# Performance work log

Hardware: AMD Instinct MI355X
Metric: run time of the kernel (lower is better)

Reference implementation:

```python
import jax, jax.numpy as jnp
import numpy as np

B, S, D_MODEL, N_HEADS = 2, 2048, 1024, 16
HEAD_DIM = D_MODEL // N_HEADS
BASE = 10000.0

# 3D RoPE slice sizes: n_pairs = head_dim//2 split into x,y,z
_n_pairs = HEAD_DIM // 2
_px = _n_pairs // 3
_py = _n_pairs // 3
_pz = _n_pairs - _px - _py
D_X, D_Y, D_Z = _px * 2, _py * 2, _pz * 2  # 20, 20, 24


def _rotate_half(x):
    # interleaved pairs: (x0,x1,x2,x3,...) -> (-x1,x0,-x3,x2,...)
    x1 = x[..., ::2]
    x2 = x[..., 1::2]
    return jnp.stack((-x2, x1), axis=-1).reshape(x.shape)


def _rope_apply(x, pos, dim):
    # x: [B,H,S,dim]; pos: [B,S] int coords
    if dim == 0:
        return x
    inv_freq = 1.0 / (BASE ** (jnp.arange(0, dim, 2, dtype=jnp.float32) / dim))
    t = pos.astype(jnp.float32)[..., None] * inv_freq          # [B,S,dim//2]
    cos = jnp.repeat(jnp.cos(t), 2, axis=-1)[:, None]          # [B,1,S,dim]
    sin = jnp.repeat(jnp.sin(t), 2, axis=-1)[:, None]
    return x * cos + _rotate_half(x) * sin


def _rope3d(q, k, pos_xyz):
    s1, s2, s3 = D_X, D_X + D_Y, D_X + D_Y + D_Z
    parts_q, parts_k = [], []
    for (a, b), ax in (((0, s1), 0), ((s1, s2), 1), ((s2, s3), 2)):
        d = b - a
        parts_q.append(_rope_apply(q[..., a:b], pos_xyz[..., ax], d))
        parts_k.append(_rope_apply(k[..., a:b], pos_xyz[..., ax], d))
    return jnp.concatenate(parts_q, axis=-1), jnp.concatenate(parts_k, axis=-1)


def setup_inputs() -> dict:
    key = jax.random.key(0)
    k1, k2, k3, k4 = jax.random.split(key, 4)
    hidden_states = jax.random.normal(k1, (B, S, D_MODEL), dtype=jnp.float32)
    # padding: each batch row keeps first `len` tokens
    lengths = jnp.array([S - 37, S - 130], dtype=jnp.int32)
    attention_mask = jnp.arange(S)[None, :] < lengths[:, None]          # [B,S] bool, True=keep
    causal_mask = jnp.triu(jnp.ones((S, S), dtype=bool), k=1)[None, None]  # True=masked
    pos_xyz = jax.random.randint(k2, (B, S, 3), 0, 30).astype(jnp.int32)
    w_qkv = jax.random.normal(k3, (3 * D_MODEL, D_MODEL), dtype=jnp.float32) * (D_MODEL ** -0.5)
    w_out = jax.random.normal(k4, (D_MODEL, D_MODEL), dtype=jnp.float32) * (D_MODEL ** -0.5)
    return {"hidden_states": hidden_states, "w_qkv": w_qkv, "w_out": w_out,
            "attention_mask": attention_mask, "causal_mask": causal_mask,
            "pos_xyz": pos_xyz}


def reference(hidden_states, w_qkv, w_out, attention_mask, causal_mask, pos_xyz):
    Bb, Ss, Dd = hidden_states.shape
    scale = HEAD_DIM ** -0.5
    qkv = jnp.einsum('bsd,ed->bse', hidden_states, w_qkv)               # [B,S,3D]
    qkv = qkv.reshape(Bb, Ss, 3, N_HEADS, HEAD_DIM).transpose(2, 0, 3, 1, 4)
    q, k, v = qkv[0], qkv[1], qkv[2]                                    # [B,H,S,hd]
    q, k = _rope3d(q, k, pos_xyz)
    scores = jnp.einsum('bhqd,bhkd->bhqk', q, k) * scale                # [B,H,S,S]
    scores = jnp.where(causal_mask, -jnp.inf, scores)
    scores = jnp.where(attention_mask[:, None, None, :], scores, -jnp.inf)
    weights = jax.nn.softmax(scores, axis=-1)                           # dropout p=0 (eval)
    out = jnp.einsum('bhqk,bhkd->bhqd', weights, v)
    out = out.transpose(0, 2, 1, 3).reshape(Bb, Ss, Dd)
    return jnp.einsum('bsd,ed->bse', out, w_out)
```

## Files before the change

### kernel.cpp

```cpp
#include <hip/hip_runtime.h>
#include <math.h>

extern "C" __device__ float __ocml_native_exp2_f32(float);

namespace {

typedef __attribute__((ext_vector_type(8))) short short8;
typedef __attribute__((ext_vector_type(4))) short short4b;
typedef __attribute__((ext_vector_type(4))) float floatx4;

constexpr int B_ = 2;
constexpr int S_ = 2048;
constexpr int DM_ = 1024;
constexpr int NH_ = 16;
constexpr int HD_ = 64;

__device__ inline unsigned short f2bf(float f) {
  unsigned u = __builtin_bit_cast(unsigned, f);
  u += 0x7fffu + ((u >> 16) & 1u);
  return (unsigned short)(u >> 16);
}

template <int CTRL>
__device__ inline float dpp_ror(float x) {
  const int r = __builtin_amdgcn_update_dpp(
      0, __builtin_bit_cast(int, x), CTRL, 0xF, 0xF, false);
  return __builtin_bit_cast(float, r);
}

__device__ inline void gl2lds16(const unsigned short* g, unsigned short* l) {
  __builtin_amdgcn_global_load_lds(
      (const __attribute__((address_space(1))) unsigned int*)g,
      (__attribute__((address_space(3))) unsigned int*)l, 16, 0, 0);
}

__global__ __launch_bounds__(256) void prep(
    const float* __restrict__ hidden, const float* __restrict__ wqkv,
    const float* __restrict__ wout, const unsigned char* __restrict__ mask,
    unsigned short* __restrict__ hb, int* __restrict__ lengths) {
  const int bid = blockIdx.x;
  if (bid < 4096) {
    const int i = bid * 256 + threadIdx.x;
    const float* src;
    int off;
    if (i < 524288)              { src = hidden; off = 0; }
    else if (i < 524288 + 393216){ src = wqkv;   off = 524288; }
    else                         { src = wout;   off = 524288 + 393216; }
    const size_t j = (size_t)(i - off);
    const float4 a = ((const float4*)src)[j * 2];
    const float4 b = ((const float4*)src)[j * 2 + 1];
    short8 v;
    v[0] = (short)f2bf(a.x); v[1] = (short)f2bf(a.y);
    v[2] = (short)f2bf(a.z); v[3] = (short)f2bf(a.w);
    v[4] = (short)f2bf(b.x); v[5] = (short)f2bf(b.y);
    v[6] = (short)f2bf(b.z); v[7] = (short)f2bf(b.w);
    ((short8*)hb)[i] = v;
  } else {
    const int b = bid - 4096;
    const int es1 = (mask[1] != 0);
    __shared__ int cnt;
    if (threadIdx.x == 0) cnt = 0;
    __syncthreads();
    int local = 0;
    for (int s = threadIdx.x; s < S_; s += blockDim.x) {
      bool nz;
      if (es1) nz = mask[b * S_ + s] != 0;
      else     nz = ((const unsigned int*)mask)[b * S_ + s] != 0;
      local += nz ? 1 : 0;
    }
    atomicAdd(&cnt, local);
    __syncthreads();
    if (threadIdx.x == 0) lengths[b] = cnt;
  }
}

__global__ __launch_bounds__(256) void qkv_gemm(
    const unsigned short* __restrict__ A, const unsigned short* __restrict__ W,
    const int* __restrict__ pos_xyz,
    unsigned short* __restrict__ Qb, unsigned short* __restrict__ Kb,
    unsigned short* __restrict__ Vtb) {
  __shared__ __align__(16) unsigned short As[128 * 32];
  __shared__ __align__(16) unsigned short Bs[128 * 32];
  const int m0 = blockIdx.y * 128, n0 = blockIdx.x * 128;
  const int w = threadIdx.x >> 6, lane = threadIdx.x & 63;
  const int lm = lane & 15, q4 = lane >> 4;
  const int srow = w * 32;
  const int r_in = lane >> 2, c_in = (lane & 3) * 8;
  const int wr = (w >> 1) * 64, wc = (w & 1) * 64;
  const int which = n0 >> 10;
  floatx4 acc[4][4];
  const floatx4 z4 = {0.f, 0.f, 0.f, 0.f};
#pragma unroll
  for (int i = 0; i < 4; i++)
#pragma unroll
    for (int j = 0; j < 4; j++) acc[i][j] = z4;

  for (int k0 = 0; k0 < DM_; k0 += 32) {
    gl2lds16(A + (size_t)(m0 + srow + r_in) * DM_ + k0 + c_in, As + srow * 32);
    gl2lds16(A + (size_t)(m0 + srow + 16 + r_in) * DM_ + k0 + c_in,
             As + (srow + 16) * 32);
    gl2lds16(W + (size_t)(n0 + srow + r_in) * DM_ + k0 + c_in, Bs + srow * 32);
    gl2lds16(W + (size_t)(n0 + srow + 16 + r_in) * DM_ + k0 + c_in,
             Bs + (srow + 16) * 32);
    __syncthreads();
    short8 af[4], bf[4];
#pragma unroll
    for (int t = 0; t < 4; t++)
      af[t] = *(const short8*)(As + (wr + t * 16 + lm) * 32 + q4 * 8);
#pragma unroll
    for (int t = 0; t < 4; t++)
      bf[t] = *(const short8*)(Bs + (wc + t * 16 + lm) * 32 + q4 * 8);
    if (which == 2) {
#pragma unroll
      for (int i = 0; i < 4; i++)
#pragma unroll
        for (int j = 0; j < 4; j++)
          acc[i][j] = __builtin_amdgcn_mfma_f32_16x16x32_bf16(af[i], bf[j],
                                                              acc[i][j], 0, 0, 0);
    } else {
#pragma unroll
      for (int i = 0; i < 4; i++)
#pragma unroll
        for (int j = 0; j < 4; j++)
          acc[i][j] = __builtin_amdgcn_mfma_f32_16x16x32_bf16(bf[i], af[j],
                                                              acc[i][j], 0, 0, 0);
    }
    __syncthreads();
  }

  const int h = ((n0 + wc) & 1023) >> 6;
  if (which == 2) {
#pragma unroll
    for (int nt = 0; nt < 4; nt++) {
      const int d = nt * 16 + lm;
#pragma unroll
      for (int mt = 0; mt < 4; mt++) {
        const int m = m0 + wr + mt * 16 + q4 * 4;
        const int bi = m >> 11, si = m & (S_ - 1);
        short4b pk;
#pragma unroll
        for (int r = 0; r < 4; r++) pk[r] = (short)f2bf(acc[mt][nt][r]);
        *(short4b*)(Vtb + ((size_t)(bi * NH_ + h) * HD_ + d) * S_ + si) = pk;
      }
    }
  } else {
    unsigned short* Dst = (which == 0) ? Qb : Kb;
    const float osc = (which == 0) ? 0.125f * 1.44269504088896f : 1.0f;
#pragma unroll
    for (int nt = 0; nt < 4; nt++) {
      const int dbase = nt * 16 + q4 * 4;
      const int p0 = dbase >> 1;
      int axis, j0, dseg;
      if (p0 < 10)      { axis = 0; j0 = p0;      dseg = 20; }
      else if (p0 < 20) { axis = 1; j0 = p0 - 10; dseg = 20; }
      else              { axis = 2; j0 = p0 - 20; dseg = 24; }
      const float invf0 =
          __expf(-(2.0f * (float)j0 / (float)dseg) * 9.210340371976184f);
      const float invf1 =
          __expf(-(2.0f * (float)(j0 + 1) / (float)dseg) * 9.210340371976184f);
#pragma unroll
      for (int mt = 0; mt < 4; mt++) {
        const int m = m0 + wr + mt * 16 + lm;
        const int bi = m >> 11, si = m & (S_ - 1);
        const int pos = pos_xyz[((size_t)bi * S_ + si) * 3 + axis];
        short4b pk;
#pragma unroll
        for (int u = 0; u < 2; u++) {
          const float ve = acc[nt][mt][2 * u], vo = acc[nt][mt][2 * u + 1];
          float sn, cs;
          sincosf((float)pos * (u ? invf1 : invf0), &sn, &cs);
          pk[2 * u]     = (short)f2bf(fmaf(ve, cs, -vo * sn) * osc);
          pk[2 * u + 1] = (short)f2bf(fmaf(vo, cs, ve * sn) * osc);
        }
        *(short4b*)(Dst + ((size_t)(bi * NH_ + h) * S_ + si) * HD_ + dbase) = pk;
      }
    }
  }
}

__global__ __launch_bounds__(256) void flash_mfma(
    const unsigned short* __restrict__ Q, const unsigned short* __restrict__ Kg,
    const unsigned short* __restrict__ Vt, const int* __restrict__ lengths,
    unsigned short* __restrict__ Oa) {
  __shared__ __align__(16) unsigned short Ks[2 * 64 * 64];
  __shared__ __align__(16) unsigned short Vs[2 * 64 * 64];
  __shared__ __align__(16) unsigned short Ps[4][16 * 64];

  const int lin = blockIdx.y * gridDim.x + blockIdx.x;
  const int xcd = lin & 7, k = lin >> 3;
  const int s = k >> 5, c = k & 31;
  const int pc = (c & 1) ? 31 - (c >> 1) : (c >> 1);
  const int qt = (s & 1) ? 31 - pc : pc;
  const int bh = xcd * 4 + s;
  const int b = bh >> 4, h = bh & 15;
  const int q0 = qt * 64;

  const int w = threadIdx.x >> 6, lane = threadIdx.x & 63;
  const int lm = lane & 15, q4 = lane >> 4;
  const int len = lengths[b];
  const unsigned short* Qp = Q + (size_t)bh * S_ * HD_;
  const unsigned short* Kp = Kg + (size_t)bh * S_ * HD_;
  const unsigned short* Vp = Vt + (size_t)bh * HD_ * S_;

  const int r8 = lane >> 3, c8 = lane & 7;
  const int rs0 = w * 16 + r8, rs1 = rs0 + 8;
  const int cs = (c8 ^ (rs0 & 7)) << 3;
  const unsigned short* gK0 = Kp + (size_t)rs0 * HD_ + cs;
  const unsigned short* gK1 = Kp + (size_t)rs1 * HD_ + cs;
  const unsigned short* gV0 = Vp + (size_t)rs0 * S_ + cs;
  const unsigned short* gV1 = Vp + (size_t)rs1 * S_ + cs;
  unsigned short* dK0 = Ks + w * 16 * 64;
  unsigned short* dK1 = Ks + (w * 16 + 8) * 64;
  unsigned short* dV0 = Vs + w * 16 * 64;
  unsigned short* dV1 = Vs + (w * 16 + 8) * 64;

  const int qrow = q0 + w * 16 + lm;
  short8 qf[2];
  qf[0] = *(const short8*)(Qp + (size_t)qrow * HD_ + q4 * 8);
  qf[1] = *(const short8*)(Qp + (size_t)qrow * HD_ + 32 + q4 * 8);

  const floatx4 z4 = {0.f, 0.f, 0.f, 0.f};
  floatx4 o[4];
#pragma unroll
  for (int dt = 0; dt < 4; dt++) o[dt] = z4;
  float m_i[4], l_i[4];
#pragma unroll
  for (int r = 0; r < 4; r++) { m_i[r] = -1e30f; l_i[r] = 0.0f; }

  unsigned short* ps = Ps[w];
  const int ktiles = min(qt + 1, (len + 63) >> 6);

  gl2lds16(gK0, dK0);
  gl2lds16(gK1, dK1);
  gl2lds16(gV0, dV0);
  gl2lds16(gV1, dV1);
  __syncthreads();

  int cur = 0;
  for (int kt = 0; kt < ktiles; kt++) {
    const int k0 = kt * 64;
    if (kt + 1 < ktiles) {
      const size_t koff = (size_t)(k0 + 64) * HD_;
      const int nb = (cur ^ 1) * 4096;
      gl2lds16(gK0 + koff, dK0 + nb);
      gl2lds16(gK1 + koff, dK1 + nb);
      gl2lds16(gV0 + (k0 + 64), dV0 + nb);
      gl2lds16(gV1 + (k0 + 64), dV1 + nb);
    }
    const unsigned short* kc = Ks + cur * 4096;
    const unsigned short* vc = Vs + cur * 4096;

    floatx4 sc[4];
    __builtin_amdgcn_s_setprio(1);
#pragma unroll
    for (int nt = 0; nt < 4; nt++) {
      const int row = nt * 16 + lm, sw = row & 7;
      const unsigned short* kb = kc + row * 64;
      const short8 b0 = *(const short8*)(kb + ((q4 ^ sw) << 3));
      const short8 b1 = *(const short8*)(kb + (((q4 + 4) ^ sw) << 3));
      sc[nt] = __builtin_amdgcn_mfma_f32_16x16x32_bf16(qf[0], b0, z4, 0, 0, 0);
      sc[nt] = __builtin_amdgcn_mfma_f32_16x16x32_bf16(qf[1], b1, sc[nt], 0, 0, 0);
    }
    __builtin_amdgcn_s_setprio(0);
    if (kt == qt || k0 + 64 > len) {
#pragma unroll
      for (int nt = 0; nt < 4; nt++) {
        const int col = k0 + nt * 16 + lm;
#pragma unroll
        for (int r = 0; r < 4; r++) {
          const int row = q0 + w * 16 + q4 * 4 + r;
          if (col > row || col >= len) sc[nt][r] = -1e30f;
        }
      }
    }
    float mx[4];
#pragma unroll
    for (int r = 0; r < 4; r++) {
      float m0 = fmaxf(fmaxf(sc[0][r], sc[1][r]), fmaxf(sc[2][r], sc[3][r]));
      m0 = fmaxf(m0, dpp_ror<0x121>(m0));
      m0 = fmaxf(m0, dpp_ror<0x122>(m0));
      m0 = fmaxf(m0, dpp_ror<0x124>(m0));
      m0 = fmaxf(m0, dpp_ror<0x128>(m0));
      mx[r] = m0;
    }
    const bool ok = (mx[0] <= m_i[0] + 8.f) && (mx[1] <= m_i[1] + 8.f) &&
                    (mx[2] <= m_i[2] + 8.f) && (mx[3] <= m_i[3] + 8.f);
    if (!__all(ok)) {
#pragma unroll
      for (int r = 0; r < 4; r++) {
        const float mt = fmaxf(m_i[r], mx[r]);
        const float al = __ocml_native_exp2_f32(m_i[r] - mt);
        l_i[r] *= al;
        m_i[r] = mt;
#pragma unroll
        for (int dt = 0; dt < 4; dt++) o[dt][r] *= al;
      }
    }
#pragma unroll
    for (int r = 0; r < 4; r++) {
      float rs = 0.0f;
#pragma unroll
      for (int nt = 0; nt < 4; nt++) {
        const float pp = __ocml_native_exp2_f32(sc[nt][r] - m_i[r]);
        sc[nt][r] = pp;
        rs += pp;
      }
      rs += dpp_ror<0x121>(rs);
      rs += dpp_ror<0x122>(rs);
      rs += dpp_ror<0x124>(rs);
      rs += dpp_ror<0x128>(rs);
      l_i[r] += rs;
    }
#pragma unroll
    for (int nt = 0; nt < 4; nt++)
#pragma unroll
      for (int r = 0; r < 4; r++) {
        const int row = q4 * 4 + r;
        const int cc = (((nt * 2 + (lm >> 3)) ^ (row & 7)) << 3) | (lm & 7);
        ps[row * 64 + cc] = f2bf(sc[nt][r]);
      }
    __builtin_amdgcn_s_setprio(1);
#pragma unroll
    for (int ks = 0; ks < 2; ks++) {
      const short8 pf = *(const short8*)(
          ps + lm * 64 + ((((ks << 2) + q4) ^ (lm & 7)) << 3));
#pragma unroll
      for (int dt = 0; dt < 4; dt++) {
        const int row = dt * 16 + lm, sw = row & 7;
        const short8 vf = *(const short8*)(
            vc + row * 64 + ((((ks << 2) + q4) ^ sw) << 3));
        o[dt] = __builtin_amdgcn_mfma_f32_16x16x32_bf16(pf, vf, o[dt], 0, 0, 0);
      }
    }
    __builtin_amdgcn_s_setprio(0);
    __syncthreads();
    cur ^= 1;
  }
  float invl[4];
#pragma unroll
  for (int r = 0; r < 4; r++) invl[r] = 1.0f / l_i[r];
#pragma unroll
  for (int dt = 0; dt < 4; dt++)
#pragma unroll
    for (int r = 0; r < 4; r++) {
      const int row = q0 + w * 16 + q4 * 4 + r;
      const int col = h * HD_ + dt * 16 + lm;
      Oa[((size_t)b * S_ + row) * DM_ + col] = f2bf(o[dt][r] * invl[r]);
    }
}

__global__ __launch_bounds__(256) void out_gemm(
    const unsigned short* __restrict__ A, const unsigned short* __restrict__ W,
    float* __restrict__ C) {
  __shared__ __align__(16) unsigned short As[128 * 32];
  __shared__ __align__(16) unsigned short Bs[128 * 32];
  const int m0 = blockIdx.y * 128, n0 = blockIdx.x * 128;
  const int w = threadIdx.x >> 6, lane = threadIdx.x & 63;
  const int lm = lane & 15, q4 = lane >> 4;
  const int srow = w * 32;
  const int r_in = lane >> 2, c_in = (lane & 3) * 8;
  const int wr = (w >> 1) * 64, wc = (w & 1) * 64;
  floatx4 acc[4][4];
  const floatx4 z4 = {0.f, 0.f, 0.f, 0.f};
#pragma unroll
  for (int i = 0; i < 4; i++)
#pragma unroll
    for (int j = 0; j < 4; j++) acc[i][j] = z4;

  for (int k0 = 0; k0 < DM_; k0 += 32) {
    gl2lds16(A + (size_t)(m0 + srow + r_in) * DM_ + k0 + c_in, As + srow * 32);
    gl2lds16(A + (size_t)(m0 + srow + 16 + r_in) * DM_ + k0 + c_in,
             As + (srow + 16) * 32);
    gl2lds16(W + (size_t)(n0 + srow + r_in) * DM_ + k0 + c_in, Bs + srow * 32);
    gl2lds16(W + (size_t)(n0 + srow + 16 + r_in) * DM_ + k0 + c_in,
             Bs + (srow + 16) * 32);
    __syncthreads();
    short8 af[4], bf[4];
#pragma unroll
    for (int t = 0; t < 4; t++)
      af[t] = *(const short8*)(As + (wr + t * 16 + lm) * 32 + q4 * 8);
#pragma unroll
    for (int t = 0; t < 4; t++)
      bf[t] = *(const short8*)(Bs + (wc + t * 16 + lm) * 32 + q4 * 8);
#pragma unroll
    for (int i = 0; i < 4; i++)
#pragma unroll
      for (int j = 0; j < 4; j++)
        acc[i][j] =
            __builtin_amdgcn_mfma_f32_16x16x32_bf16(bf[i], af[j], acc[i][j],
                                                    0, 0, 0);
    __syncthreads();
  }
#pragma unroll
  for (int nt = 0; nt < 4; nt++) {
    const int nbase = n0 + wc + nt * 16 + q4 * 4;
#pragma unroll
    for (int mt = 0; mt < 4; mt++) {
      const int m = m0 + wr + mt * 16 + lm;
      *(floatx4*)(C + (size_t)m * DM_ + nbase) = acc[nt][mt];
    }
  }
}

}

extern "C" void kernel_launch(void* const* d_in, const int* in_sizes, int n_in,
                              void* d_out, int out_size, void* d_ws, size_t ws_size,
                              hipStream_t stream) {
  const float* hidden = (const float*)d_in[0];
  const float* w_qkv = (const float*)d_in[1];
  const float* w_out = (const float*)d_in[2];
  const unsigned char* amask = (const unsigned char*)d_in[3];
  const int* pos_xyz = (const int*)d_in[5];
  float* out = (float*)d_out;

  constexpr size_t NHID = (size_t)B_ * S_ * DM_;
  constexpr size_t NWQ = (size_t)3 * DM_ * DM_;
  constexpr size_t NWO = (size_t)DM_ * DM_;
  constexpr size_t NQKV = (size_t)B_ * NH_ * S_ * HD_;

  unsigned short* hb = (unsigned short*)d_ws;
  unsigned short* wqb = hb + NHID;
  unsigned short* wob = wqb + NWQ;
  unsigned short* Qb = wob + NWO;
  unsigned short* Kb = Qb + NQKV;
  unsigned short* Vtb = Kb + NQKV;
  unsigned short* attn = Vtb + NQKV;
  int* lens = (int*)(attn + NQKV);

  prep<<<dim3(4096 + B_), dim3(256), 0, stream>>>(hidden, w_qkv, w_out, amask,
                                                  hb, lens);
  qkv_gemm<<<dim3(3 * DM_ / 128, B_ * S_ / 128), dim3(256), 0, stream>>>(
      hb, wqb, pos_xyz, Qb, Kb, Vtb);
  flash_mfma<<<dim3(S_ / 64, B_ * NH_), dim3(256), 0, stream>>>(
      Qb, Kb, Vtb, lens, attn);
  out_gemm<<<dim3(DM_ / 128, B_ * S_ / 128), dim3(256), 0, stream>>>(
      attn, wob, out);
}
```

Before: 240.5 us.

## Double-buffer LDS tiles and XOR-swizzle layout in QKV and output GEMMs

Both projection GEMMs now keep two LDS buffers, so the global-to-LDS copy for the next K slice is issued before the MFMAs run on the current slice. This replaces the previous load, sync, compute pattern and aims to hide global load latency behind compute. The column chunk within each 32-element row is also XOR-swizzled by a row-dependent factor, on both the store and the fragment reads, to cut LDS bank conflicts. LDS use doubles per block, which may lower occupancy.

```diff
diff --git a/kernel.cpp b/kernel.cpp
--- a/kernel.cpp
+++ b/kernel.cpp
@@ -79,15 +79,17 @@
     const int* __restrict__ pos_xyz,
     unsigned short* __restrict__ Qb, unsigned short* __restrict__ Kb,
     unsigned short* __restrict__ Vtb) {
-  __shared__ __align__(16) unsigned short As[128 * 32];
-  __shared__ __align__(16) unsigned short Bs[128 * 32];
+  __shared__ __align__(16) unsigned short As[2 * 128 * 32];
+  __shared__ __align__(16) unsigned short Bs[2 * 128 * 32];
   const int m0 = blockIdx.y * 128, n0 = blockIdx.x * 128;
   const int w = threadIdx.x >> 6, lane = threadIdx.x & 63;
   const int lm = lane & 15, q4 = lane >> 4;
   const int srow = w * 32;
-  const int r_in = lane >> 2, c_in = (lane & 3) * 8;
+  const int r_in = lane >> 2;
+  const int c_sw = (((lane & 3) ^ ((r_in >> 1) & 3)) << 3);
   const int wr = (w >> 1) * 64, wc = (w & 1) * 64;
   const int which = n0 >> 10;
+  const int rsw = (lm >> 1) & 3;
   floatx4 acc[4][4];
   const floatx4 z4 = {0.f, 0.f, 0.f, 0.f};
 #pragma unroll
@@ -95,21 +97,35 @@
 #pragma unroll
     for (int j = 0; j < 4; j++) acc[i][j] = z4;
 
+  const unsigned short* gA0 = A + (size_t)(m0 + srow + r_in) * DM_ + c_sw;
+  const unsigned short* gA1 = A + (size_t)(m0 + srow + 16 + r_in) * DM_ + c_sw;
+  const unsigned short* gB0 = W + (size_t)(n0 + srow + r_in) * DM_ + c_sw;
+  const unsigned short* gB1 = W + (size_t)(n0 + srow + 16 + r_in) * DM_ + c_sw;
+
+  gl2lds16(gA0, As + srow * 32);
+  gl2lds16(gA1, As + (srow + 16) * 32);
+  gl2lds16(gB0, Bs + srow * 32);
+  gl2lds16(gB1, Bs + (srow + 16) * 32);
+  __syncthreads();
+
+  int cur = 0;
   for (int k0 = 0; k0 < DM_; k0 += 32) {
-    gl2lds16(A + (size_t)(m0 + srow + r_in) * DM_ + k0 + c_in, As + srow * 32);
-    gl2lds16(A + (size_t)(m0 + srow + 16 + r_in) * DM_ + k0 + c_in,
-             As + (srow + 16) * 32);
-    gl2lds16(W + (size_t)(n0 + srow + r_in) * DM_ + k0 + c_in, Bs + srow * 32);
-    gl2lds16(W + (size_t)(n0 + srow + 16 + r_in) * DM_ + k0 + c_in,
-             Bs + (srow + 16) * 32);
-    __syncthreads();
+    if (k0 + 32 < DM_) {
+      const int nb = (cur ^ 1) * 4096;
+      gl2lds16(gA0 + k0 + 32, As + nb + srow * 32);
+      gl2lds16(gA1 + k0 + 32, As + nb + (srow + 16) * 32);
+      gl2lds16(gB0 + k0 + 32, Bs + nb + srow * 32);
+      gl2lds16(gB1 + k0 + 32, Bs + nb + (srow + 16) * 32);
+    }
+    const unsigned short* as = As + cur * 4096;
+    const unsigned short* bs = Bs + cur * 4096;
     short8 af[4], bf[4];
 #pragma unroll
     for (int t = 0; t < 4; t++)
-      af[t] = *(const short8*)(As + (wr + t * 16 + lm) * 32 + q4 * 8);
+      af[t] = *(const short8*)(as + (wr + t * 16 + lm) * 32 + ((q4 ^ rsw) << 3));
 #pragma unroll
     for (int t = 0; t < 4; t++)
-      bf[t] = *(const short8*)(Bs + (wc + t * 16 + lm) * 32 + q4 * 8);
+      bf[t] = *(const short8*)(bs + (wc + t * 16 + lm) * 32 + ((q4 ^ rsw) << 3));
     if (which == 2) {
 #pragma unroll
       for (int i = 0; i < 4; i++)
@@ -126,6 +142,7 @@
                                                               acc[i][j], 0, 0, 0);
     }
     __syncthreads();
+    cur ^= 1;
   }
 
   const int h = ((n0 + wc) & 1023) >> 6;
@@ -352,14 +369,16 @@
 __global__ __launch_bounds__(256) void out_gemm(
     const unsigned short* __restrict__ A, const unsigned short* __restrict__ W,
     float* __restrict__ C) {
-  __shared__ __align__(16) unsigned short As[128 * 32];
-  __shared__ __align__(16) unsigned short Bs[128 * 32];
+  __shared__ __align__(16) unsigned short As[2 * 128 * 32];
+  __shared__ __align__(16) unsigned short Bs[2 * 128 * 32];
   const int m0 = blockIdx.y * 128, n0 = blockIdx.x * 128;
   const int w = threadIdx.x >> 6, lane = threadIdx.x & 63;
   const int lm = lane & 15, q4 = lane >> 4;
   const int srow = w * 32;
-  const int r_in = lane >> 2, c_in = (lane & 3) * 8;
+  const int r_in = lane >> 2;
+  const int c_sw = (((lane & 3) ^ ((r_in >> 1) & 3)) << 3);
   const int wr = (w >> 1) * 64, wc = (w & 1) * 64;
+  const int rsw = (lm >> 1) & 3;
   floatx4 acc[4][4];
   const floatx4 z4 = {0.f, 0.f, 0.f, 0.f};
 #pragma unroll
@@ -367,21 +386,35 @@
 #pragma unroll
     for (int j = 0; j < 4; j++) acc[i][j] = z4;
 
+  const unsigned short* gA0 = A + (size_t)(m0 + srow + r_in) * DM_ + c_sw;
+  const unsigned short* gA1 = A + (size_t)(m0 + srow + 16 + r_in) * DM_ + c_sw;
+  const unsigned short* gB0 = W + (size_t)(n0 + srow + r_in) * DM_ + c_sw;
+  const unsigned short* gB1 = W + (size_t)(n0 + srow + 16 + r_in) * DM_ + c_sw;
+
+  gl2lds16(gA0, As + srow * 32);
+  gl2lds16(gA1, As + (srow + 16) * 32);
+  gl2lds16(gB0, Bs + srow * 32);
+  gl2lds16(gB1, Bs + (srow + 16) * 32);
+  __syncthreads();
+
+  int cur = 0;
   for (int k0 = 0; k0 < DM_; k0 += 32) {
-    gl2lds16(A + (size_t)(m0 + srow + r_in) * DM_ + k0 + c_in, As + srow * 32);
-    gl2lds16(A + (size_t)(m0 + srow + 16 + r_in) * DM_ + k0 + c_in,
-             As + (srow + 16) * 32);
-    gl2lds16(W + (size_t)(n0 + srow + r_in) * DM_ + k0 + c_in, Bs + srow * 32);
-    gl2lds16(W + (size_t)(n0 + srow + 16 + r_in) * DM_ + k0 + c_in,
-             Bs + (srow + 16) * 32);
-    __syncthreads();
+    if (k0 + 32 < DM_) {
+      const int nb = (cur ^ 1) * 4096;
+      gl2lds16(gA0 + k0 + 32, As + nb + srow * 32);
+      gl2lds16(gA1 + k0 + 32, As + nb + (srow + 16) * 32);
+      gl2lds16(gB0 + k0 + 32, Bs + nb + srow * 32);
+      gl2lds16(gB1 + k0 + 32, Bs + nb + (srow + 16) * 32);
+    }
+    const unsigned short* as = As + cur * 4096;
+    const unsigned short* bs = Bs + cur * 4096;
     short8 af[4], bf[4];
 #pragma unroll
     for (int t = 0; t < 4; t++)
-      af[t] = *(const short8*)(As + (wr + t * 16 + lm) * 32 + q4 * 8);
+      af[t] = *(const short8*)(as + (wr + t * 16 + lm) * 32 + ((q4 ^ rsw) << 3));
 #pragma unroll
     for (int t = 0; t < 4; t++)
-      bf[t] = *(const short8*)(Bs + (wc + t * 16 + lm) * 32 + q4 * 8);
+      bf[t] = *(const short8*)(bs + (wc + t * 16 + lm) * 32 + ((q4 ^ rsw) << 3));
 #pragma unroll
     for (int i = 0; i < 4; i++)
 #pragma unroll
@@ -390,6 +423,7 @@
             __builtin_amdgcn_mfma_f32_16x16x32_bf16(bf[i], af[j], acc[i][j],
                                                     0, 0, 0);
     __syncthreads();
+    cur ^= 1;
   }
 #pragma unroll
   for (int nt = 0; nt < 4; nt++) {
```

Measured after the change: 238.0 us. No clear change (-1.0%).
